# Optimization experiments

Measured on AMD Instinct MI355X. Metric: run time of the kernel, lower is better.

## Reference

```python
import jax, jax.numpy as jnp
import numpy as np

B, N, K = 2, 1024, 512
I, O = 16, 64
RADIUS = 1.0


def setup_inputs() -> dict:
    key = jax.random.key(0)
    ks = jax.random.split(key, 24)

    def w(k, fi, fo):
        return (jax.random.normal(k, (fi, fo), jnp.float32) / np.float32(np.sqrt(fi)))

    def b(k, fo):
        return jax.random.normal(k, (fo,), jnp.float32) * 0.01

    return {
        "positions": jax.random.normal(ks[0], (B, N, 3), jnp.float32),
        "features": jax.random.normal(ks[1], (B, N, I), jnp.float32),
        "sa0_w1": w(ks[2], I + 3, O), "sa0_b1": b(ks[3], O),
        "sa0_w2": w(ks[4], O, O), "sa0_b2": b(ks[5], O),
        "sa1_w1": w(ks[6], O + 3, O), "sa1_b1": b(ks[7], O),
        "sa1_w2": w(ks[8], O, O), "sa1_b2": b(ks[9], O),
        "lin0_w1": w(ks[10], O, O), "lin0_b1": b(ks[11], O),
        "lin0_w2": w(ks[12], O, O), "lin0_b2": b(ks[13], O),
        "lin1_w1": w(ks[14], O, O), "lin1_b1": b(ks[15], O),
        "lin1_w2": w(ks[16], O, O), "lin1_b2": b(ks[17], O),
        "lt0_w": w(ks[18], I, O), "lt0_b": b(ks[19], O),
        "lt1_w": w(ks[20], O, O), "lt1_b": b(ks[21], O),
    }


def _ball_query(xyz, k, radius):
    # pytorch3d ball_query semantics: first k in-radius neighbors in index
    # order, padded with -1. We return clamped idx + validity mask.
    d2 = jnp.sum((xyz[:, :, None, :] - xyz[:, None, :, :]) ** 2, axis=-1)  # [B,N,N]
    n = xyz.shape[1]
    ar = jnp.arange(n)
    keymat = jnp.where(d2 < radius * radius, ar[None, None, :], n)
    sk = jnp.sort(keymat, axis=-1)[..., :k]  # first k in-radius indices
    mask = sk < n
    idx = jnp.where(mask, sk, 0)
    return idx, mask


def _gather(points, idx):
    # points [B,N,C], idx [B,S,K] -> [B,S,K,C]
    return jax.vmap(lambda p, i: p[i])(points, idx)


def _sa_module(feats, xyz, idx, mask, w1, b1, w2, b2):
    grouped_xyz = _gather(xyz, idx) - xyz[:, :, None, :]        # [B,N,K,3]
    grouped_pts = _gather(feats, idx)                            # [B,N,K,C]
    h = jnp.concatenate([grouped_xyz, grouped_pts], axis=-1)     # [B,N,K,C+3]
    h = jax.nn.leaky_relu(h @ w1 + b1, 0.2)
    h = jax.nn.leaky_relu(h @ w2 + b2, 0.2)
    h = h * mask[..., None].astype(h.dtype)
    return jnp.max(h, axis=2)                                    # [B,N,O]


def reference(positions, features,
              sa0_w1, sa0_b1, sa0_w2, sa0_b2,
              sa1_w1, sa1_b1, sa1_w2, sa1_b2,
              lin0_w1, lin0_b1, lin0_w2, lin0_b2,
              lin1_w1, lin1_b1, lin1_w2, lin1_b2,
              lt0_w, lt0_b, lt1_w, lt1_b):
    # ratio == 1.0 -> new_xyz == xyz for every layer; neighbor idx is shared.
    idx, mask = _ball_query(positions, K, RADIUS)

    # layer 0
    x_i = _sa_module(features, positions, idx, mask, sa0_w1, sa0_b1, sa0_w2, sa0_b2)
    x_i = jax.nn.relu(x_i @ lin0_w1 + lin0_b1) @ lin0_w2 + lin0_b2
    x = features @ lt0_w + lt0_b + x_i

    # layer 1
    x_i = _sa_module(x, positions, idx, mask, sa1_w1, sa1_b1, sa1_w2, sa1_b2)
    x_i = jax.nn.relu(x_i @ lin1_w1 + lin1_b1) @ lin1_w2 + lin1_b2
    x = x @ lt1_w + lt1_b + x_i
    return x
```

## Files before the change

kernel.cpp:

```cpp
#include <hip/hip_runtime.h>
#include <cstdint>
#include <cfloat>

#define BB 2
#define NN 1024
#define KK 512
#define II 16
#define OO 64
#define R2 1.0f
#define PTOT (BB * NN)

typedef __attribute__((ext_vector_type(8))) short short8;
typedef __attribute__((ext_vector_type(4))) float f32x4;

__device__ __forceinline__ float lrelu(float v) { return v > 0.0f ? v : 0.2f * v; }

__device__ __forceinline__ unsigned short f2bf(float f) {
    unsigned int x = __float_as_uint(f);
    return (unsigned short)((x + 0x7fffu + ((x >> 16) & 1u)) >> 16);
}
__device__ __forceinline__ float bf2f(unsigned short h) {
    return __uint_as_float(((unsigned int)h) << 16);
}

__global__ __launch_bounds__(256) void setup_k(
    const float* __restrict__ pos, const float* __restrict__ feat,
    const float* __restrict__ w1, const float* __restrict__ b1,
    const float* __restrict__ w2l0, const float* __restrict__ w2l1,
    unsigned short* __restrict__ idx, int* __restrict__ cnt,
    float* __restrict__ g, float* __restrict__ t,
    unsigned short* __restrict__ bh0, unsigned short* __restrict__ bl0,
    unsigned short* __restrict__ bh1, unsigned short* __restrict__ bl1)
{
    const int wave = threadIdx.x >> 6;
    const int lane = threadIdx.x & 63;

    if (blockIdx.x < PTOT / 4) {
        const int p = blockIdx.x * 4 + wave;
        const int b = p >> 10;
        const float cx = pos[p * 3 + 0];
        const float cy = pos[p * 3 + 1];
        const float cz = pos[p * 3 + 2];
        const float* pb = pos + (size_t)b * NN * 3;
        unsigned short* op = idx + (size_t)p * KK;
        int count = 0;
        for (int jb = 0; jb < NN; jb += 64) {
            const int j = jb + lane;
            const float dx = pb[j * 3 + 0] - cx;
            const float dy = pb[j * 3 + 1] - cy;
            const float dz = pb[j * 3 + 2] - cz;
            const float d2 = dx * dx + dy * dy + dz * dz;
            const bool pred = d2 < R2;
            const unsigned long long m = __ballot(pred);
            const int before = __popcll(m & ((1ull << lane) - 1ull));
            const int w = count + before;
            if (pred && w < KK) op[w] = (unsigned short)j;
            count += __popcll(m);
        }
        if (lane == 0) cnt[p] = count;
    } else if (blockIdx.x < PTOT / 2) {
        const int p = (blockIdx.x - PTOT / 4) * 4 + wave;
        const int c = lane;
        const float px = pos[p * 3 + 0];
        const float py = pos[p * 3 + 1];
        const float pz = pos[p * 3 + 2];
        const float s = px * w1[0 * 64 + c] + py * w1[1 * 64 + c] + pz * w1[2 * 64 + c];
        float acc = b1[c] + s;
        const float* f = feat + (size_t)p * II;
#pragma unroll
        for (int q = 0; q < II; ++q)
            acc = fmaf(f[q], w1[(3 + q) * 64 + c], acc);
        g[(size_t)p * 64 + c] = acc;
        t[(size_t)p * 64 + c] = s;
    } else {
        const int layer = blockIdx.x - PTOT / 2;
        const float* src = layer == 0 ? w2l0 : w2l1;
        unsigned short* dh = layer == 0 ? bh0 : bh1;
        unsigned short* dl = layer == 0 ? bl0 : bl1;
#pragma unroll
        for (int i = 0; i < 2; ++i) {
            const int e = threadIdx.x * 2 + i;
            const int kf = e >> 8;
            const int ct = (e >> 6) & 3;
            const int ln = e & 63;
            const int kg = ln >> 4;
            const int rw = ln & 15;
#pragma unroll
            for (int j = 0; j < 8; ++j) {
                const float w = src[(kf * 32 + kg * 8 + j) * 64 + ct * 16 + rw];
                const unsigned short h = f2bf(w);
                dh[(size_t)e * 8 + j] = h;
                dl[(size_t)e * 8 + j] = f2bf(w - bf2f(h));
            }
        }
    }
}

template <int CB, bool LAST>
__global__ __launch_bounds__(256) void sa_fused_k(
    const float* __restrict__ g, const float* __restrict__ t,
    const unsigned short* __restrict__ idx, const int* __restrict__ cnt,
    const unsigned short* __restrict__ bhws, const unsigned short* __restrict__ blws,
    const float* __restrict__ b2,
    const float* __restrict__ wa, const float* __restrict__ ba,
    const float* __restrict__ wb, const float* __restrict__ bbias,
    const float* __restrict__ wc, const float* __restrict__ bc,
    const float* __restrict__ base, const float* __restrict__ pos,
    const float* __restrict__ w1n, const float* __restrict__ b1n,
    float* __restrict__ xout, float* __restrict__ gn, float* __restrict__ tn)
{
    const int p = blockIdx.x;
    const int lane = threadIdx.x & 63;
    const int wave = threadIdx.x >> 6;
    const int b = p >> 10;
    const int row = lane & 15;
    const int kg  = lane >> 4;

    const short8* bhp = (const short8*)bhws;
    const short8* blp = (const short8*)blws;
    short8 bh[2][4], bl[2][4];
#pragma unroll
    for (int kf = 0; kf < 2; ++kf)
#pragma unroll
        for (int ct = 0; ct < 4; ++ct) {
            bh[kf][ct] = bhp[(kf * 4 + ct) * 64 + lane];
            bl[kf][ct] = blp[(kf * 4 + ct) * 64 + lane];
        }

    float b2v[4];
#pragma unroll
    for (int ct = 0; ct < 4; ++ct) b2v[ct] = b2[ct * 16 + row];

    const float* tp = t + (size_t)p * 64 + kg * 8;
    const float4 tva = *(const float4*)tp;
    const float4 tvb = *(const float4*)(tp + 4);
    const float4 tvc = *(const float4*)(tp + 32);
    const float4 tvd = *(const float4*)(tp + 36);
    const float tv0[8] = {tva.x, tva.y, tva.z, tva.w, tvb.x, tvb.y, tvb.z, tvb.w};
    const float tv1[8] = {tvc.x, tvc.y, tvc.z, tvc.w, tvd.x, tvd.y, tvd.z, tvd.w};

    const int craw = cnt[p];
    const int vc = craw < KK ? craw : KK;
    const unsigned short* mi = idx + (size_t)p * KK;
    const float* gbp = g + (size_t)b * NN * 64;

    float lmaxv[4] = {-FLT_MAX, -FLT_MAX, -FLT_MAX, -FLT_MAX};
    const int ntiles = (vc + 15) >> 4;

    for (int tile = wave; tile < ntiles; tile += 4) {
        const int j16 = tile * 16 + row;
        const int jc = j16 < vc ? j16 : vc - 1;
        const int jidx = (int)mi[jc];
        const float* grow = gbp + (size_t)jidx * 64 + kg * 8;
        const float4 ga = *(const float4*)grow;
        const float4 gb2 = *(const float4*)(grow + 4);
        const float4 gc = *(const float4*)(grow + 32);
        const float4 gd = *(const float4*)(grow + 36);
        const float v0[8] = {ga.x, ga.y, ga.z, ga.w, gb2.x, gb2.y, gb2.z, gb2.w};
        const float v1[8] = {gc.x, gc.y, gc.z, gc.w, gd.x, gd.y, gd.z, gd.w};

        short8 ah0, al0, ah1, al1;
#pragma unroll
        for (int j = 0; j < 8; ++j) {
            const float h1a = lrelu(v0[j] - tv0[j]);
            const unsigned short ha = f2bf(h1a);
            ah0[j] = (short)ha;
            al0[j] = (short)f2bf(h1a - bf2f(ha));
            const float h1b = lrelu(v1[j] - tv1[j]);
            const unsigned short hb = f2bf(h1b);
            ah1[j] = (short)hb;
            al1[j] = (short)f2bf(h1b - bf2f(hb));
        }

#pragma unroll
        for (int ct = 0; ct < 4; ++ct) {
            f32x4 a = {0.0f, 0.0f, 0.0f, 0.0f};
            a = __builtin_amdgcn_mfma_f32_16x16x32_bf16(ah0, bh[0][ct], a, 0, 0, 0);
            a = __builtin_amdgcn_mfma_f32_16x16x32_bf16(al0, bh[0][ct], a, 0, 0, 0);
            a = __builtin_amdgcn_mfma_f32_16x16x32_bf16(ah0, bl[0][ct], a, 0, 0, 0);
            a = __builtin_amdgcn_mfma_f32_16x16x32_bf16(ah1, bh[1][ct], a, 0, 0, 0);
            a = __builtin_amdgcn_mfma_f32_16x16x32_bf16(al1, bh[1][ct], a, 0, 0, 0);
            a = __builtin_amdgcn_mfma_f32_16x16x32_bf16(ah1, bl[1][ct], a, 0, 0, 0);
#pragma unroll
            for (int r = 0; r < 4; ++r) {
                const int nb = tile * 16 + kg * 4 + r;
                const float h2 = lrelu(a[r] + b2v[ct]);
                lmaxv[ct] = fmaxf(lmaxv[ct], nb < vc ? h2 : 0.0f);
            }
        }
    }

    __shared__ float red[4][64];
#pragma unroll
    for (int ct = 0; ct < 4; ++ct) {
        lmaxv[ct] = fmaxf(lmaxv[ct], __shfl_xor(lmaxv[ct], 16));
        lmaxv[ct] = fmaxf(lmaxv[ct], __shfl_xor(lmaxv[ct], 32));
    }
    if (lane < 16) {
#pragma unroll
        for (int ct = 0; ct < 4; ++ct) red[wave][ct * 16 + lane] = lmaxv[ct];
    }
    __syncthreads();

    if (wave == 0) {
        float m = fmaxf(fmaxf(red[0][lane], red[1][lane]),
                        fmaxf(red[2][lane], red[3][lane]));
        if (craw < KK) m = fmaxf(m, 0.0f);

        float a0 = ba[lane], a1 = 0.0f, a2 = 0.0f, a3 = 0.0f;
#pragma unroll
        for (int o = 0; o < 64; o += 4) {
            a0 = fmaf(__shfl(m, o + 0), wa[(o + 0) * 64 + lane], a0);
            a1 = fmaf(__shfl(m, o + 1), wa[(o + 1) * 64 + lane], a1);
            a2 = fmaf(__shfl(m, o + 2), wa[(o + 2) * 64 + lane], a2);
            a3 = fmaf(__shfl(m, o + 3), wa[(o + 3) * 64 + lane], a3);
        }
        const float tmp = fmaxf((a0 + a1) + (a2 + a3), 0.0f);

        float e0 = bbias[lane], e1 = 0.0f, e2 = 0.0f, e3 = 0.0f;
#pragma unroll
        for (int o = 0; o < 64; o += 4) {
            e0 = fmaf(__shfl(tmp, o + 0), wb[(o + 0) * 64 + lane], e0);
            e1 = fmaf(__shfl(tmp, o + 1), wb[(o + 1) * 64 + lane], e1);
            e2 = fmaf(__shfl(tmp, o + 2), wb[(o + 2) * 64 + lane], e2);
            e3 = fmaf(__shfl(tmp, o + 3), wb[(o + 3) * 64 + lane], e3);
        }
        const float xi = (e0 + e1) + (e2 + e3);

        float r0 = bc[lane], r1 = 0.0f, r2 = 0.0f, r3 = 0.0f;
        const float* bp = base + (size_t)p * CB;
#pragma unroll
        for (int f = 0; f < CB; f += 4) {
            r0 = fmaf(bp[f + 0], wc[(f + 0) * 64 + lane], r0);
            r1 = fmaf(bp[f + 1], wc[(f + 1) * 64 + lane], r1);
            r2 = fmaf(bp[f + 2], wc[(f + 2) * 64 + lane], r2);
            r3 = fmaf(bp[f + 3], wc[(f + 3) * 64 + lane], r3);
        }
        const float xv = ((r0 + r1) + (r2 + r3)) + xi;
        xout[(size_t)p * 64 + lane] = xv;

        if constexpr (!LAST) {
            const float px = pos[p * 3 + 0];
            const float py = pos[p * 3 + 1];
            const float pz = pos[p * 3 + 2];
            const float s = px * w1n[0 * 64 + lane] + py * w1n[1 * 64 + lane]
                          + pz * w1n[2 * 64 + lane];
            float g0 = b1n[lane] + s, g1v = 0.0f, g2 = 0.0f, g3 = 0.0f;
#pragma unroll
            for (int q = 0; q < 64; q += 4) {
                g0  = fmaf(__shfl(xv, q + 0), w1n[(3 + q + 0) * 64 + lane], g0);
                g1v = fmaf(__shfl(xv, q + 1), w1n[(3 + q + 1) * 64 + lane], g1v);
                g2  = fmaf(__shfl(xv, q + 2), w1n[(3 + q + 2) * 64 + lane], g2);
                g3  = fmaf(__shfl(xv, q + 3), w1n[(3 + q + 3) * 64 + lane], g3);
            }
            gn[(size_t)p * 64 + lane] = (g0 + g1v) + (g2 + g3);
            tn[(size_t)p * 64 + lane] = s;
        }
    }
}

extern "C" void kernel_launch(void* const* d_in, const int* in_sizes, int n_in,
                              void* d_out, int out_size, void* d_ws, size_t ws_size,
                              hipStream_t stream)
{
    const float* positions = (const float*)d_in[0];
    const float* features  = (const float*)d_in[1];
    const float* sa0_w1 = (const float*)d_in[2];
    const float* sa0_b1 = (const float*)d_in[3];
    const float* sa0_w2 = (const float*)d_in[4];
    const float* sa0_b2 = (const float*)d_in[5];
    const float* sa1_w1 = (const float*)d_in[6];
    const float* sa1_b1 = (const float*)d_in[7];
    const float* sa1_w2 = (const float*)d_in[8];
    const float* sa1_b2 = (const float*)d_in[9];
    const float* lin0_w1 = (const float*)d_in[10];
    const float* lin0_b1 = (const float*)d_in[11];
    const float* lin0_w2 = (const float*)d_in[12];
    const float* lin0_b2 = (const float*)d_in[13];
    const float* lin1_w1 = (const float*)d_in[14];
    const float* lin1_b1 = (const float*)d_in[15];
    const float* lin1_w2 = (const float*)d_in[16];
    const float* lin1_b2 = (const float*)d_in[17];
    const float* lt0_w = (const float*)d_in[18];
    const float* lt0_b = (const float*)d_in[19];
    const float* lt1_w = (const float*)d_in[20];
    const float* lt1_b = (const float*)d_in[21];

    const int P = PTOT;

    unsigned short* idx = (unsigned short*)d_ws;
    int* cnt = (int*)(idx + (size_t)P * KK);
    float* g0 = (float*)(cnt + P);
    float* t0 = g0 + (size_t)P * OO;
    float* g1 = t0 + (size_t)P * OO;
    float* t1 = g1 + (size_t)P * OO;
    float* x  = t1 + (size_t)P * OO;
    unsigned short* bh0 = (unsigned short*)(x + (size_t)P * OO);
    unsigned short* bl0 = bh0 + 4096;
    unsigned short* bh1 = bl0 + 4096;
    unsigned short* bl1 = bh1 + 4096;

    float* out = (float*)d_out;

    setup_k<<<P / 2 + 2, 256, 0, stream>>>(positions, features, sa0_w1, sa0_b1,
                                           sa0_w2, sa1_w2,
                                           idx, cnt, g0, t0, bh0, bl0, bh1, bl1);

    sa_fused_k<II, false><<<P, 256, 0, stream>>>(
        g0, t0, idx, cnt, bh0, bl0, sa0_b2,
        lin0_w1, lin0_b1, lin0_w2, lin0_b2, lt0_w, lt0_b,
        features, positions, sa1_w1, sa1_b1, x, g1, t1);

    sa_fused_k<OO, true><<<P, 256, 0, stream>>>(
        g1, t1, idx, cnt, bh1, bl1, sa1_b2,
        lin1_w1, lin1_b1, lin1_w2, lin1_b2, lt1_w, lt1_b,
        x, positions, nullptr, nullptr, out, nullptr, nullptr);
}
```

Baseline: 159.1 us.

## Map one point per wave, prefetch neighbor gathers, merge setup phases

The layer kernels now give each wave its own point instead of splitting one point's neighbor tiles across four waves. This removes the shared-memory max reduction and __syncthreads, and lets all four waves run the MLP tail instead of only wave 0 doing it while the others idle. The neighbor-tile loop software-prefetches the next tile's gathered rows into registers so global loads overlap with the MFMA work. Setup folds the g/t projection into the ball-query waves, which reuses the loaded center coordinates and halves the block count. The risk is fewer blocks (512) and per-wave load imbalance from varying neighbor counts, plus more register pressure from the prefetch buffers.

```diff
diff --git a/kernel.cpp b/kernel.cpp
--- a/kernel.cpp
+++ b/kernel.cpp
@@ -9,6 +9,7 @@
 #define OO 64
 #define R2 1.0f
 #define PTOT (BB * NN)
+#define PBLK (PTOT / 4)
 
 typedef __attribute__((ext_vector_type(8))) short short8;
 typedef __attribute__((ext_vector_type(4))) float f32x4;
@@ -35,7 +36,7 @@
     const int wave = threadIdx.x >> 6;
     const int lane = threadIdx.x & 63;
 
-    if (blockIdx.x < PTOT / 4) {
+    if (blockIdx.x < PBLK) {
         const int p = blockIdx.x * 4 + wave;
         const int b = p >> 10;
         const float cx = pos[p * 3 + 0];
@@ -58,13 +59,8 @@
             count += __popcll(m);
         }
         if (lane == 0) cnt[p] = count;
-    } else if (blockIdx.x < PTOT / 2) {
-        const int p = (blockIdx.x - PTOT / 4) * 4 + wave;
         const int c = lane;
-        const float px = pos[p * 3 + 0];
-        const float py = pos[p * 3 + 1];
-        const float pz = pos[p * 3 + 2];
-        const float s = px * w1[0 * 64 + c] + py * w1[1 * 64 + c] + pz * w1[2 * 64 + c];
+        const float s = cx * w1[0 * 64 + c] + cy * w1[1 * 64 + c] + cz * w1[2 * 64 + c];
         float acc = b1[c] + s;
         const float* f = feat + (size_t)p * II;
 #pragma unroll
@@ -73,7 +69,7 @@
         g[(size_t)p * 64 + c] = acc;
         t[(size_t)p * 64 + c] = s;
     } else {
-        const int layer = blockIdx.x - PTOT / 2;
+        const int layer = blockIdx.x - PBLK;
         const float* src = layer == 0 ? w2l0 : w2l1;
         unsigned short* dh = layer == 0 ? bh0 : bh1;
         unsigned short* dl = layer == 0 ? bl0 : bl1;
@@ -97,7 +93,7 @@
 }
 
 template <int CB, bool LAST>
-__global__ __launch_bounds__(256) void sa_fused_k(
+__global__ __launch_bounds__(256) void layer_k(
     const float* __restrict__ g, const float* __restrict__ t,
     const unsigned short* __restrict__ idx, const int* __restrict__ cnt,
     const unsigned short* __restrict__ bhws, const unsigned short* __restrict__ blws,
@@ -109,9 +105,9 @@
     const float* __restrict__ w1n, const float* __restrict__ b1n,
     float* __restrict__ xout, float* __restrict__ gn, float* __restrict__ tn)
 {
-    const int p = blockIdx.x;
     const int lane = threadIdx.x & 63;
     const int wave = threadIdx.x >> 6;
+    const int p = blockIdx.x * 4 + wave;
     const int b = p >> 10;
     const int row = lane & 15;
     const int kg  = lane >> 4;
@@ -147,18 +143,27 @@
     float lmaxv[4] = {-FLT_MAX, -FLT_MAX, -FLT_MAX, -FLT_MAX};
     const int ntiles = (vc + 15) >> 4;
 
-    for (int tile = wave; tile < ntiles; tile += 4) {
-        const int j16 = tile * 16 + row;
-        const int jc = j16 < vc ? j16 : vc - 1;
-        const int jidx = (int)mi[jc];
-        const float* grow = gbp + (size_t)jidx * 64 + kg * 8;
-        const float4 ga = *(const float4*)grow;
-        const float4 gb2 = *(const float4*)(grow + 4);
-        const float4 gc = *(const float4*)(grow + 32);
-        const float4 gd = *(const float4*)(grow + 36);
-        const float v0[8] = {ga.x, ga.y, ga.z, ga.w, gb2.x, gb2.y, gb2.z, gb2.w};
-        const float v1[8] = {gc.x, gc.y, gc.z, gc.w, gd.x, gd.y, gd.z, gd.w};
-
+    int jc = row < vc ? row : vc - 1;
+    const float* grow = gbp + (size_t)mi[jc] * 64 + kg * 8;
+    float4 ca = *(const float4*)grow;
+    float4 cb = *(const float4*)(grow + 4);
+    float4 cc = *(const float4*)(grow + 32);
+    float4 cd = *(const float4*)(grow + 36);
+
+    for (int tile = 0; tile < ntiles; ++tile) {
+        float4 na, nb4, nc, nd;
+        if (tile + 1 < ntiles) {
+            const int j16 = (tile + 1) * 16 + row;
+            const int jn = j16 < vc ? j16 : vc - 1;
+            const float* nrow = gbp + (size_t)mi[jn] * 64 + kg * 8;
+            na = *(const float4*)nrow;
+            nb4 = *(const float4*)(nrow + 4);
+            nc = *(const float4*)(nrow + 32);
+            nd = *(const float4*)(nrow + 36);
+        }
+
+        const float v0[8] = {ca.x, ca.y, ca.z, ca.w, cb.x, cb.y, cb.z, cb.w};
+        const float v1[8] = {cc.x, cc.y, cc.z, cc.w, cd.x, cd.y, cd.z, cd.w};
         short8 ah0, al0, ah1, al1;
 #pragma unroll
         for (int j = 0; j < 8; ++j) {
@@ -188,74 +193,69 @@
                 lmaxv[ct] = fmaxf(lmaxv[ct], nb < vc ? h2 : 0.0f);
             }
         }
-    }
-
-    __shared__ float red[4][64];
+        ca = na; cb = nb4; cc = nc; cd = nd;
+    }
+
 #pragma unroll
     for (int ct = 0; ct < 4; ++ct) {
         lmaxv[ct] = fmaxf(lmaxv[ct], __shfl_xor(lmaxv[ct], 16));
         lmaxv[ct] = fmaxf(lmaxv[ct], __shfl_xor(lmaxv[ct], 32));
     }
-    if (lane < 16) {
-#pragma unroll
-        for (int ct = 0; ct < 4; ++ct) red[wave][ct * 16 + lane] = lmaxv[ct];
-    }
-    __syncthreads();
-
-    if (wave == 0) {
-        float m = fmaxf(fmaxf(red[0][lane], red[1][lane]),
-                        fmaxf(red[2][lane], red[3][lane]));
-        if (craw < KK) m = fmaxf(m, 0.0f);
-
-        float a0 = ba[lane], a1 = 0.0f, a2 = 0.0f, a3 = 0.0f;
-#pragma unroll
-        for (int o = 0; o < 64; o += 4) {
-            a0 = fmaf(__shfl(m, o + 0), wa[(o + 0) * 64 + lane], a0);
-            a1 = fmaf(__shfl(m, o + 1), wa[(o + 1) * 64 + lane], a1);
-            a2 = fmaf(__shfl(m, o + 2), wa[(o + 2) * 64 + lane], a2);
-            a3 = fmaf(__shfl(m, o + 3), wa[(o + 3) * 64 + lane], a3);
-        }
-        const float tmp = fmaxf((a0 + a1) + (a2 + a3), 0.0f);
-
-        float e0 = bbias[lane], e1 = 0.0f, e2 = 0.0f, e3 = 0.0f;
-#pragma unroll
-        for (int o = 0; o < 64; o += 4) {
-            e0 = fmaf(__shfl(tmp, o + 0), wb[(o + 0) * 64 + lane], e0);
-            e1 = fmaf(__shfl(tmp, o + 1), wb[(o + 1) * 64 + lane], e1);
-            e2 = fmaf(__shfl(tmp, o + 2), wb[(o + 2) * 64 + lane], e2);
-            e3 = fmaf(__shfl(tmp, o + 3), wb[(o + 3) * 64 + lane], e3);
-        }
-        const float xi = (e0 + e1) + (e2 + e3);
-
-        float r0 = bc[lane], r1 = 0.0f, r2 = 0.0f, r3 = 0.0f;
-        const float* bp = base + (size_t)p * CB;
-#pragma unroll
-        for (int f = 0; f < CB; f += 4) {
-            r0 = fmaf(bp[f + 0], wc[(f + 0) * 64 + lane], r0);
-            r1 = fmaf(bp[f + 1], wc[(f + 1) * 64 + lane], r1);
-            r2 = fmaf(bp[f + 2], wc[(f + 2) * 64 + lane], r2);
-            r3 = fmaf(bp[f + 3], wc[(f + 3) * 64 + lane], r3);
-        }
-        const float xv = ((r0 + r1) + (r2 + r3)) + xi;
-        xout[(size_t)p * 64 + lane] = xv;
-
-        if constexpr (!LAST) {
-            const float px = pos[p * 3 + 0];
-            const float py = pos[p * 3 + 1];
-            const float pz = pos[p * 3 + 2];
-            const float s = px * w1n[0 * 64 + lane] + py * w1n[1 * 64 + lane]
-                          + pz * w1n[2 * 64 + lane];
-            float g0 = b1n[lane] + s, g1v = 0.0f, g2 = 0.0f, g3 = 0.0f;
-#pragma unroll
-            for (int q = 0; q < 64; q += 4) {
-                g0  = fmaf(__shfl(xv, q + 0), w1n[(3 + q + 0) * 64 + lane], g0);
-                g1v = fmaf(__shfl(xv, q + 1), w1n[(3 + q + 1) * 64 + lane], g1v);
-                g2  = fmaf(__shfl(xv, q + 2), w1n[(3 + q + 2) * 64 + lane], g2);
-                g3  = fmaf(__shfl(xv, q + 3), w1n[(3 + q + 3) * 64 + lane], g3);
-            }
-            gn[(size_t)p * 64 + lane] = (g0 + g1v) + (g2 + g3);
-            tn[(size_t)p * 64 + lane] = s;
-        }
+    const float s0 = __shfl(lmaxv[0], row);
+    const float s1 = __shfl(lmaxv[1], row);
+    const float s2 = __shfl(lmaxv[2], row);
+    const float s3 = __shfl(lmaxv[3], row);
+    float m = lane < 16 ? s0 : lane < 32 ? s1 : lane < 48 ? s2 : s3;
+    if (craw < KK) m = fmaxf(m, 0.0f);
+
+    float a0 = ba[lane], a1 = 0.0f, a2 = 0.0f, a3 = 0.0f;
+#pragma unroll
+    for (int o = 0; o < 64; o += 4) {
+        a0 = fmaf(__shfl(m, o + 0), wa[(o + 0) * 64 + lane], a0);
+        a1 = fmaf(__shfl(m, o + 1), wa[(o + 1) * 64 + lane], a1);
+        a2 = fmaf(__shfl(m, o + 2), wa[(o + 2) * 64 + lane], a2);
+        a3 = fmaf(__shfl(m, o + 3), wa[(o + 3) * 64 + lane], a3);
+    }
+    const float tmp = fmaxf((a0 + a1) + (a2 + a3), 0.0f);
+
+    float e0 = bbias[lane], e1 = 0.0f, e2 = 0.0f, e3 = 0.0f;
+#pragma unroll
+    for (int o = 0; o < 64; o += 4) {
+        e0 = fmaf(__shfl(tmp, o + 0), wb[(o + 0) * 64 + lane], e0);
+        e1 = fmaf(__shfl(tmp, o + 1), wb[(o + 1) * 64 + lane], e1);
+        e2 = fmaf(__shfl(tmp, o + 2), wb[(o + 2) * 64 + lane], e2);
+        e3 = fmaf(__shfl(tmp, o + 3), wb[(o + 3) * 64 + lane], e3);
+    }
+    const float xi = (e0 + e1) + (e2 + e3);
+
+    float r0 = bc[lane], r1 = 0.0f, r2 = 0.0f, r3 = 0.0f;
+    const float* bp = base + (size_t)p * CB;
+#pragma unroll
+    for (int f = 0; f < CB; f += 4) {
+        r0 = fmaf(bp[f + 0], wc[(f + 0) * 64 + lane], r0);
+        r1 = fmaf(bp[f + 1], wc[(f + 1) * 64 + lane], r1);
+        r2 = fmaf(bp[f + 2], wc[(f + 2) * 64 + lane], r2);
+        r3 = fmaf(bp[f + 3], wc[(f + 3) * 64 + lane], r3);
+    }
+    const float xv = ((r0 + r1) + (r2 + r3)) + xi;
+    xout[(size_t)p * 64 + lane] = xv;
+
+    if constexpr (!LAST) {
+        const float px = pos[p * 3 + 0];
+        const float py = pos[p * 3 + 1];
+        const float pz = pos[p * 3 + 2];
+        const float s = px * w1n[0 * 64 + lane] + py * w1n[1 * 64 + lane]
+                      + pz * w1n[2 * 64 + lane];
+        float g0 = b1n[lane] + s, g1v = 0.0f, g2 = 0.0f, g3 = 0.0f;
+#pragma unroll
+        for (int q = 0; q < 64; q += 4) {
+            g0  = fmaf(__shfl(xv, q + 0), w1n[(3 + q + 0) * 64 + lane], g0);
+            g1v = fmaf(__shfl(xv, q + 1), w1n[(3 + q + 1) * 64 + lane], g1v);
+            g2  = fmaf(__shfl(xv, q + 2), w1n[(3 + q + 2) * 64 + lane], g2);
+            g3  = fmaf(__shfl(xv, q + 3), w1n[(3 + q + 3) * 64 + lane], g3);
+        }
+        gn[(size_t)p * 64 + lane] = (g0 + g1v) + (g2 + g3);
+        tn[(size_t)p * 64 + lane] = s;
     }
 }
 
@@ -302,16 +302,16 @@
 
     float* out = (float*)d_out;
 
-    setup_k<<<P / 2 + 2, 256, 0, stream>>>(positions, features, sa0_w1, sa0_b1,
-                                           sa0_w2, sa1_w2,
-                                           idx, cnt, g0, t0, bh0, bl0, bh1, bl1);
-
-    sa_fused_k<II, false><<<P, 256, 0, stream>>>(
+    setup_k<<<PBLK + 2, 256, 0, stream>>>(positions, features, sa0_w1, sa0_b1,
+                                          sa0_w2, sa1_w2,
+                                          idx, cnt, g0, t0, bh0, bl0, bh1, bl1);
+
+    layer_k<II, false><<<PBLK, 256, 0, stream>>>(
         g0, t0, idx, cnt, bh0, bl0, sa0_b2,
         lin0_w1, lin0_b1, lin0_w2, lin0_b2, lt0_w, lt0_b,
         features, positions, sa1_w1, sa1_b1, x, g1, t1);
 
-    sa_fused_k<OO, true><<<P, 256, 0, stream>>>(
+    layer_k<OO, true><<<PBLK, 256, 0, stream>>>(
         g1, t1, idx, cnt, bh1, bl1, sa1_b2,
         lin1_w1, lin1_b1, lin1_w2, lin1_b2, lt1_w, lt1_b,
         x, positions, nullptr, nullptr, out, nullptr, nullptr);
```

New measurement: 151.2 us, median of 2. 1.05x faster.
